# Kernel tuning notes

Hardware: AMD Instinct MI355X
Metric: run time of the kernel (lower is better)

The kernel has to match this reference:

```python
import jax, jax.numpy as jnp
import numpy as np
from jax import lax

T = 4096  # time length; conv widths 4094->1023->255->84 (even) so view(-1,30) works

def relu6(v):
    return jnp.clip(v, 0.0, 6.0)

def setup_inputs() -> dict:
    key = jax.random.key(0)
    ks = jax.random.split(key, 20)
    s = 0.25  # ~ torch default init scale for fan_in 16
    x = jax.random.normal(ks[0], (1, 1, 18, T), dtype=jnp.float32)
    # 4 stacked Linear(16,16) per cross-modal block: [Q, Kin, Vin, QKVout]
    cm1_W = jax.random.normal(ks[1], (4, 16, 16), dtype=jnp.float32) * s
    cm1_b = jax.random.normal(ks[2], (4, 16), dtype=jnp.float32) * s
    cm2_W = jax.random.normal(ks[3], (4, 16, 16), dtype=jnp.float32) * s
    cm2_b = jax.random.normal(ks[4], (4, 16), dtype=jnp.float32) * s
    cw0 = jax.random.normal(ks[5], (5, 1, 2, 3), dtype=jnp.float32) * 0.3
    cw1 = jax.random.normal(ks[6], (5, 5, 2, 4), dtype=jnp.float32) * 0.15
    cw2 = jax.random.normal(ks[7], (5, 5, 2, 4), dtype=jnp.float32) * 0.15
    cw3 = jax.random.normal(ks[8], (5, 5, 2, 4), dtype=jnp.float32) * 0.15
    cb = jax.random.normal(ks[9], (4, 5), dtype=jnp.float32) * 0.1
    fc1_W = jax.random.normal(ks[10], (15, 30), dtype=jnp.float32) * 0.18
    fc1_b = jax.random.normal(ks[11], (15,), dtype=jnp.float32) * 0.18
    fc2_W = jax.random.normal(ks[12], (2, 15), dtype=jnp.float32) * 0.25
    fc2_b = jax.random.normal(ks[13], (2,), dtype=jnp.float32) * 0.25
    return dict(x=x, cm1_W=cm1_W, cm1_b=cm1_b, cm2_W=cm2_W, cm2_b=cm2_b,
                cw0=cw0, cw1=cw1, cw2=cw2, cw3=cw3, cb=cb,
                fc1_W=fc1_W, fc1_b=fc1_b, fc2_W=fc2_W, fc2_b=fc2_b)

def _cm(wav_row, eeg2, W, b):
    # wav_row: [T], eeg2: [16, T]; W: [4,16,16], b: [4,16]
    wavP = wav_row[None, :] * eeg2          # [16, T]   (wav * eeg broadcast)
    mat = eeg2.T @ wavP                     # [T, T]
    wavP = wavP @ mat                       # [16, T]
    w = wavP.T                              # [T, 16]
    e = eeg2.T                              # [T, 16]
    Q = relu6(e @ W[0].T + b[0])            # [T, 16]
    K = relu6(w @ W[1].T + b[1])
    V = relu6(w @ W[2].T + b[2])
    # Softmax2d on [T,T,1,1] == softmax over axis 1 (per-row over keys)
    A = jax.nn.softmax(Q @ K.T, axis=1)     # [T, T]
    # Softmax2d on [T,16,1,1] == softmax over the 16 features per row
    S = jax.nn.softmax(A @ V, axis=1)       # [T, 16]
    out = relu6(S @ W[3].T + b[3])          # [T, 16]
    return out.T                            # [16, T]

def reference(x, cm1_W, cm1_b, cm2_W, cm2_b, cw0, cw1, cw2, cw3, cb,
              fc1_W, fc1_b, fc2_W, fc2_b):
    eeg2 = x[0, 0, 1:-1, :]                 # [16, T]
    wavA = _cm(x[0, 0, 0, :], eeg2, cm1_W, cm1_b)   # [16, T]
    wavB = _cm(x[0, 0, -1, :], eeg2, cm2_W, cm2_b)  # [16, T]
    y = jnp.concatenate([wavA, eeg2, wavB], axis=0)[None, None]  # [1,1,48,T]
    dn = ('NCHW', 'OIHW', 'NCHW')
    y = relu6(lax.conv_general_dilated(y, cw0, (2, 1), 'VALID', dimension_numbers=dn) + cb[0][None, :, None, None])
    y = relu6(lax.conv_general_dilated(y, cw1, (2, 4), 'VALID', dimension_numbers=dn) + cb[1][None, :, None, None])
    y = relu6(lax.conv_general_dilated(y, cw2, (2, 4), 'VALID', dimension_numbers=dn) + cb[2][None, :, None, None])
    y = relu6(lax.conv_general_dilated(y, cw3, (2, 3), 'VALID', dimension_numbers=dn) + cb[3][None, :, None, None])
    y = y.reshape(-1, 30)                   # [42, 30]
    h = jax.nn.sigmoid(y @ fc1_W.T + fc1_b) # [42, 15]
    out = jax.nn.softmax(h @ fc2_W.T + fc2_b, axis=1)  # [42, 2]
    return out
```

## Files before the change

kernel.cpp:

```cpp
#include <hip/hip_runtime.h>

#define TT 4096
#define KS 8

#define OFF_GPART 0
#define OFF_QH    32768
#define OFF_QL    98304
#define OFF_KH    163840
#define OFF_KL    229376
#define OFF_VT    294912
#define OFF_Y     360448
#define OFF_P     557056
#define OFF_C1    557056
#define OFF_C2    618496

typedef __attribute__((ext_vector_type(8))) short short8;
typedef __attribute__((ext_vector_type(4))) float f32x4;

__device__ __forceinline__ float relu6f(float v){ return fminf(fmaxf(v, 0.f), 6.f); }
__device__ __forceinline__ unsigned short f2bf(float f){
  unsigned int u = __float_as_uint(f);
  return (unsigned short)((u + 0x7FFFu + ((u>>16)&1u)) >> 16);
}
__device__ __forceinline__ float bf2f(unsigned short s){
  return __uint_as_float(((unsigned int)s)<<16);
}

__global__ __launch_bounds__(256) void k_gpart(const float* __restrict__ x, float* __restrict__ ws){
  const int b = blockIdx.x, tid = threadIdx.x;
  const int i = tid >> 4, j = tid & 15;
  const int t0 = b*64;
  const float4* ei4 = reinterpret_cast<const float4*>(x + (size_t)(1+i)*TT + t0);
  const float4* ej4 = reinterpret_cast<const float4*>(x + (size_t)(1+j)*TT + t0);
  const float4* wA4 = reinterpret_cast<const float4*>(x + t0);
  const float4* wB4 = reinterpret_cast<const float4*>(x + (size_t)17*TT + t0);
  float gA = 0.f, gB = 0.f;
  #pragma unroll 4
  for (int u = 0; u < 16; ++u){
    float4 a = ei4[u], c = ej4[u], wa = wA4[u], wb = wB4[u];
    float p0 = a.x*c.x, p1 = a.y*c.y, p2 = a.z*c.z, p3 = a.w*c.w;
    gA = fmaf(wa.x, p0, gA); gA = fmaf(wa.y, p1, gA); gA = fmaf(wa.z, p2, gA); gA = fmaf(wa.w, p3, gA);
    gB = fmaf(wb.x, p0, gB); gB = fmaf(wb.y, p1, gB); gB = fmaf(wb.z, p2, gB); gB = fmaf(wb.w, p3, gB);
  }
  ws[OFF_GPART + (size_t)tid*64 + b]         = gA;
  ws[OFF_GPART + (size_t)(256+tid)*64 + b]   = gB;
}

__global__ __launch_bounds__(128) void k_qkv(const float* __restrict__ x,
    const float* __restrict__ cm1W, const float* __restrict__ cm1b,
    const float* __restrict__ cm2W, const float* __restrict__ cm2b,
    float* __restrict__ ws){
  __shared__ float4 sG4[64];
  __shared__ float4 sW0[64], sW1[64], sW2[64];
  __shared__ float sB[48];
  const int b = blockIdx.x;
  const int cm = b >> 5;
  const int tid = threadIdx.x;
  {
    const float4* g4a = reinterpret_cast<const float4*>(ws + OFF_GPART + (size_t)(cm*256 + tid)*64);
    const float4* g4b = reinterpret_cast<const float4*>(ws + OFF_GPART + (size_t)(cm*256 + 128 + tid)*64);
    float g0 = 0.f, g1 = 0.f;
    #pragma unroll
    for (int u = 0; u < 16; ++u){
      float4 a = g4a[u], c = g4b[u];
      g0 += (a.x + a.y) + (a.z + a.w);
      g1 += (c.x + c.y) + (c.z + c.w);
    }
    ((float*)sG4)[tid]       = g0;
    ((float*)sG4)[tid + 128] = g1;
  }
  const float* W  = cm ? cm2W : cm1W;
  const float* Bb = cm ? cm2b : cm1b;
  ((float*)sW0)[tid]       = W[tid];
  ((float*)sW0)[tid + 128] = W[tid + 128];
  ((float*)sW1)[tid]       = W[256 + tid];
  ((float*)sW1)[tid + 128] = W[384 + tid];
  ((float*)sW2)[tid]       = W[512 + tid];
  ((float*)sW2)[tid + 128] = W[640 + tid];
  if (tid < 48) sB[tid] = Bb[tid];
  __syncthreads();

  const int t = (b & 31)*128 + tid;
  float e[16], p[16], w2[16];
  const float wav = x[(size_t)(cm ? 17 : 0)*TT + t];
  #pragma unroll
  for (int d = 0; d < 16; ++d){ e[d] = x[(size_t)(1+d)*TT + t]; p[d] = wav * e[d]; }

  #pragma unroll
  for (int c = 0; c < 16; ++c){
    float a = 0.f;
    #pragma unroll
    for (int dv = 0; dv < 4; ++dv){
      float4 gv = sG4[c*4+dv];
      a = fmaf(gv.x, p[4*dv+0], a); a = fmaf(gv.y, p[4*dv+1], a);
      a = fmaf(gv.z, p[4*dv+2], a); a = fmaf(gv.w, p[4*dv+3], a);
    }
    w2[c] = a;
  }
  float q[16], kk[16], vv[16];
  #pragma unroll
  for (int c = 0; c < 16; ++c){
    float aq = sB[c], ak = sB[16+c], av = sB[32+c];
    #pragma unroll
    for (int dv = 0; dv < 4; ++dv){
      float4 w0 = sW0[c*4+dv], w1 = sW1[c*4+dv], w3 = sW2[c*4+dv];
      aq = fmaf(w0.x, e[4*dv+0], aq);  aq = fmaf(w0.y, e[4*dv+1], aq);
      aq = fmaf(w0.z, e[4*dv+2], aq);  aq = fmaf(w0.w, e[4*dv+3], aq);
      ak = fmaf(w1.x, w2[4*dv+0], ak); ak = fmaf(w1.y, w2[4*dv+1], ak);
      ak = fmaf(w1.z, w2[4*dv+2], ak); ak = fmaf(w1.w, w2[4*dv+3], ak);
      av = fmaf(w3.x, w2[4*dv+0], av); av = fmaf(w3.y, w2[4*dv+1], av);
      av = fmaf(w3.z, w2[4*dv+2], av); av = fmaf(w3.w, w2[4*dv+3], av);
    }
    q[c] = relu6f(aq); kk[c] = relu6f(ak); vv[c] = relu6f(av);
  }
  unsigned short qhv[16], qlv[16], khv[16], klv[16];
  #pragma unroll
  for (int d = 0; d < 16; ++d){
    qhv[d] = f2bf(q[d]);  qlv[d] = f2bf(q[d]  - bf2f(qhv[d]));
    khv[d] = f2bf(kk[d]); klv[d] = f2bf(kk[d] - bf2f(khv[d]));
  }
  const size_t rowus = ((size_t)cm*TT + t)*16;
  unsigned int wq[8];
  #pragma unroll
  for (int xx = 0; xx < 8; ++xx) wq[xx] = (unsigned int)qhv[2*xx] | ((unsigned int)qhv[2*xx+1]<<16);
  ((uint4*)((unsigned short*)(ws+OFF_QH)+rowus))[0] = make_uint4(wq[0],wq[1],wq[2],wq[3]);
  ((uint4*)((unsigned short*)(ws+OFF_QH)+rowus))[1] = make_uint4(wq[4],wq[5],wq[6],wq[7]);
  #pragma unroll
  for (int xx = 0; xx < 8; ++xx) wq[xx] = (unsigned int)qlv[2*xx] | ((unsigned int)qlv[2*xx+1]<<16);
  ((uint4*)((unsigned short*)(ws+OFF_QL)+rowus))[0] = make_uint4(wq[0],wq[1],wq[2],wq[3]);
  ((uint4*)((unsigned short*)(ws+OFF_QL)+rowus))[1] = make_uint4(wq[4],wq[5],wq[6],wq[7]);
  #pragma unroll
  for (int xx = 0; xx < 8; ++xx) wq[xx] = (unsigned int)khv[2*xx] | ((unsigned int)khv[2*xx+1]<<16);
  ((uint4*)((unsigned short*)(ws+OFF_KH)+rowus))[0] = make_uint4(wq[0],wq[1],wq[2],wq[3]);
  ((uint4*)((unsigned short*)(ws+OFF_KH)+rowus))[1] = make_uint4(wq[4],wq[5],wq[6],wq[7]);
  #pragma unroll
  for (int xx = 0; xx < 8; ++xx) wq[xx] = (unsigned int)klv[2*xx] | ((unsigned int)klv[2*xx+1]<<16);
  ((uint4*)((unsigned short*)(ws+OFF_KL)+rowus))[0] = make_uint4(wq[0],wq[1],wq[2],wq[3]);
  ((uint4*)((unsigned short*)(ws+OFF_KL)+rowus))[1] = make_uint4(wq[4],wq[5],wq[6],wq[7]);
  unsigned short* vtp = (unsigned short*)(ws+OFF_VT) + (size_t)cm*16*TT;
  #pragma unroll
  for (int d = 0; d < 16; ++d) vtp[(size_t)d*TT + t] = f2bf(vv[d]);

  if (cm == 0){
    #pragma unroll
    for (int d = 0; d < 16; ++d) ws[OFF_Y + (size_t)(16+d)*TT + t] = e[d];
  }
}

__global__ __launch_bounds__(256) void k_attn_main(float* __restrict__ ws){
  const int unit = blockIdx.x*4 + (threadIdx.x >> 6);
  const int lane = threadIdx.x & 63;
  const int cm = unit >> 10;
  const int rem = unit & 1023;
  const int qt2 = rem >> 3;
  const int ks = rem & 7;
  const int i = lane & 15, g = lane >> 4;
  const int gb = (g & 1) * 8;

  const unsigned short* qh = (const unsigned short*)(ws + OFF_QH) + (size_t)cm*TT*16;
  const unsigned short* ql = (const unsigned short*)(ws + OFF_QL) + (size_t)cm*TT*16;
  const unsigned short* kh = (const unsigned short*)(ws + OFF_KH) + (size_t)cm*TT*16;
  const unsigned short* kl = (const unsigned short*)(ws + OFF_KL) + (size_t)cm*TT*16;
  const unsigned short* vt = (const unsigned short*)(ws + OFF_VT) + (size_t)cm*16*TT;
  const unsigned short* kbase = (g < 2) ? kh : kl;

  const int qA = qt2*32 + i, qB = qA + 16;
  const short8 b1A = *(const short8*)(qh + (size_t)qA*16 + gb);
  const short8 b2A = *(const short8*)(ql + (size_t)qA*16 + gb);
  const short8 b1B = *(const short8*)(qh + (size_t)qB*16 + gb);
  const short8 b2B = *(const short8*)(ql + (size_t)qB*16 + gb);

  const int key0 = ks*512;
  const int keyA = ((i>>2)<<3) + (i&3);
  f32x4 accA = {0.f,0.f,0.f,0.f}, accB = {0.f,0.f,0.f,0.f};
  float lsumA = 0.f, lsumB = 0.f;

  for (int t = 0; t < 16; ++t){
    const int k0 = key0 + t*32;
    const short8 a0 = *(const short8*)(kbase + ((size_t)(k0 + keyA))*16 + gb);
    const short8 a1 = *(const short8*)(kbase + ((size_t)(k0 + keyA + 4))*16 + gb);
    f32x4 d0A = {0.f,0.f,0.f,0.f}, d1A = {0.f,0.f,0.f,0.f};
    f32x4 d0B = {0.f,0.f,0.f,0.f}, d1B = {0.f,0.f,0.f,0.f};
    d0A = __builtin_amdgcn_mfma_f32_16x16x32_bf16(a0, b1A, d0A, 0,0,0);
    d0A = __builtin_amdgcn_mfma_f32_16x16x32_bf16(a0, b2A, d0A, 0,0,0);
    d1A = __builtin_amdgcn_mfma_f32_16x16x32_bf16(a1, b1A, d1A, 0,0,0);
    d1A = __builtin_amdgcn_mfma_f32_16x16x32_bf16(a1, b2A, d1A, 0,0,0);
    d0B = __builtin_amdgcn_mfma_f32_16x16x32_bf16(a0, b1B, d0B, 0,0,0);
    d0B = __builtin_amdgcn_mfma_f32_16x16x32_bf16(a0, b2B, d0B, 0,0,0);
    d1B = __builtin_amdgcn_mfma_f32_16x16x32_bf16(a1, b1B, d1B, 0,0,0);
    d1B = __builtin_amdgcn_mfma_f32_16x16x32_bf16(a1, b2B, d1B, 0,0,0);
    float p0A[4], p1A[4], p0B[4], p1B[4];
    #pragma unroll
    for (int r = 0; r < 4; ++r){
      p0A[r] = __expf(fminf(d0A[r],100.f) - 32.f); lsumA += p0A[r];
      p1A[r] = __expf(fminf(d1A[r],100.f) - 32.f); lsumA += p1A[r];
      p0B[r] = __expf(fminf(d0B[r],100.f) - 32.f); lsumB += p0B[r];
      p1B[r] = __expf(fminf(d1B[r],100.f) - 32.f); lsumB += p1B[r];
    }
    short8 paA, paB;
    #pragma unroll
    for (int r = 0; r < 4; ++r){
      paA[r]   = (short)f2bf(p0A[r]);
      paA[r+4] = (short)f2bf(p1A[r]);
      paB[r]   = (short)f2bf(p0B[r]);
      paB[r+4] = (short)f2bf(p1B[r]);
    }
    const short8 bv = *(const short8*)(vt + (size_t)i*TT + k0 + g*8);
    accA = __builtin_amdgcn_mfma_f32_16x16x32_bf16(paA, bv, accA, 0,0,0);
    accB = __builtin_amdgcn_mfma_f32_16x16x32_bf16(paB, bv, accB, 0,0,0);
  }
  lsumA += __shfl_xor(lsumA, 16);  lsumA += __shfl_xor(lsumA, 32);
  lsumB += __shfl_xor(lsumB, 16);  lsumB += __shfl_xor(lsumB, 32);
  float* Pb = ws + OFF_P + (size_t)((cm*KS + ks)*17)*TT;
  if (lane < 16){
    Pb[qt2*32 + lane]      = lsumA;
    Pb[qt2*32 + 16 + lane] = lsumB;
  }
  #pragma unroll
  for (int r = 0; r < 4; ++r){
    Pb[(size_t)(1 + i)*TT + qt2*32 + g*4 + r]      = accA[r];
    Pb[(size_t)(1 + i)*TT + qt2*32 + 16 + g*4 + r] = accB[r];
  }
}

__device__ __forceinline__ float sum8(const float* __restrict__ p){
  const size_t PL = (size_t)17*TT;
  float s0 = p[0],      s1 = p[PL],   s2 = p[2*PL], s3 = p[3*PL];
  float s4 = p[4*PL],   s5 = p[5*PL], s6 = p[6*PL], s7 = p[7*PL];
  return ((s0+s1)+(s2+s3)) + ((s4+s5)+(s6+s7));
}

__global__ __launch_bounds__(256) void k_attn_fin(
    const float* __restrict__ cm1W, const float* __restrict__ cm1b,
    const float* __restrict__ cm2W, const float* __restrict__ cm2b,
    float* __restrict__ ws){
  const int gid = blockIdx.x*256 + threadIdx.x;
  const int cm = gid >> 12;
  const int q = gid & 4095;
  const float* Pb = ws + OFF_P + (size_t)cm*KS*17*TT + q;
  const float lt = sum8(Pb);
  float a[16];
  #pragma unroll
  for (int d = 0; d < 16; ++d) a[d] = sum8(Pb + (size_t)(1+d)*TT);
  const float invl = 1.f/lt;
  float mx = -1e30f;
  #pragma unroll
  for (int d = 0; d < 16; ++d){ a[d] *= invl; mx = fmaxf(mx, a[d]); }
  float es = 0.f;
  #pragma unroll
  for (int d = 0; d < 16; ++d){ a[d] = __expf(a[d]-mx); es += a[d]; }
  const float invs = 1.f/es;
  const float* W  = cm ? cm2W : cm1W;
  const float* Bb = cm ? cm2b : cm1b;
  #pragma unroll
  for (int c = 0; c < 16; ++c){
    float o = 0.f;
    #pragma unroll
    for (int d = 0; d < 16; ++d) o = fmaf(W[768 + c*16 + d], a[d], o);
    o = relu6f(fmaf(o, invs, Bb[48 + c]));
    ws[OFF_Y + (size_t)((cm ? 32 : 0) + c)*TT + q] = o;
  }
}

__global__ __launch_bounds__(256) void k_conv01(const float* __restrict__ cw0,
    const float* __restrict__ cw1, const float* __restrict__ cb, float* __restrict__ ws){
  const int idx = blockIdx.x*256 + threadIdx.x;
  const int WO = 1023, HO = 12;
  if (idx >= 5*HO*WO) return;
  const int ow = idx % WO; int tmp = idx / WO;
  const int oh = tmp % HO; const int oc = tmp / HO;
  const float* y = ws + OFF_Y;
  float yp[4][7];
  #pragma unroll
  for (int r = 0; r < 4; ++r){
    const float* yr = y + (size_t)(4*oh + r)*TT + 4*ow;
    #pragma unroll
    for (int cx = 0; cx < 7; ++cx) yp[r][cx] = yr[cx];
  }
  float a = cb[5 + oc];
  #pragma unroll
  for (int ic = 0; ic < 5; ++ic){
    const float* w0 = cw0 + ic*6;
    const float* w1 = cw1 + ((oc*5+ic)*2)*4;
    #pragma unroll
    for (int kh = 0; kh < 2; ++kh){
      #pragma unroll
      for (int kw = 0; kw < 4; ++kw){
        float c0 = cb[ic];
        c0 = fmaf(w0[0], yp[2*kh][kw],   c0);
        c0 = fmaf(w0[1], yp[2*kh][kw+1], c0);
        c0 = fmaf(w0[2], yp[2*kh][kw+2], c0);
        c0 = fmaf(w0[3], yp[2*kh+1][kw],   c0);
        c0 = fmaf(w0[4], yp[2*kh+1][kw+1], c0);
        c0 = fmaf(w0[5], yp[2*kh+1][kw+2], c0);
        c0 = relu6f(c0);
        a = fmaf(w1[kh*4+kw], c0, a);
      }
    }
  }
  ws[OFF_C1 + idx] = relu6f(a);
}

__global__ __launch_bounds__(256) void k_conv2(const float* __restrict__ cw2,
    const float* __restrict__ cb, float* __restrict__ ws){
  const int idx = blockIdx.x*256 + threadIdx.x;
  if (idx >= 5*6*255) return;
  const int ow = idx % 255; int tmp = idx/255;
  const int oh = tmp % 6; const int oc = tmp/6;
  const float* c1 = ws + OFF_C1;
  float a = cb[10 + oc];
  #pragma unroll
  for (int ic = 0; ic < 5; ++ic)
    #pragma unroll
    for (int kh = 0; kh < 2; ++kh)
      #pragma unroll
      for (int kw = 0; kw < 4; ++kw)
        a = fmaf(cw2[((oc*5+ic)*2+kh)*4+kw], c1[(size_t)(ic*12 + 2*oh+kh)*1023 + 4*ow+kw], a);
  ws[OFF_C2 + idx] = relu6f(a);
}

__global__ __launch_bounds__(256) void k_tail(
    const float* __restrict__ cw3, const float* __restrict__ cb,
    const float* __restrict__ fc1W, const float* __restrict__ fc1b,
    const float* __restrict__ fc2W, const float* __restrict__ fc2b,
    const float* __restrict__ ws, float* __restrict__ out){
  __shared__ float c2[5*6*255];
  __shared__ float c3[5*3*84];
  __shared__ float hsm[42*15];
  const int tid = threadIdx.x;
  {
    const float4* src4 = reinterpret_cast<const float4*>(ws + OFF_C2);
    float4* c24 = reinterpret_cast<float4*>(c2);
    for (int i = tid; i < 1912; i += 256) c24[i] = src4[i];
    if (tid < 2) c2[7648 + tid] = ws[OFF_C2 + 7648 + tid];
  }
  __syncthreads();
  for (int idx = tid; idx < 5*3*84; idx += 256){
    const int ow = idx % 84; int tmp = idx/84;
    const int oh = tmp % 3; const int oc = tmp/3;
    float a = cb[15 + oc];
    #pragma unroll
    for (int ic = 0; ic < 5; ++ic)
      #pragma unroll
      for (int kh = 0; kh < 2; ++kh)
        #pragma unroll
        for (int kw = 0; kw < 4; ++kw)
          a = fmaf(cw3[((oc*5+ic)*2+kh)*4+kw], c2[(ic*6 + 2*oh+kh)*255 + 3*ow+kw], a);
    c3[idx] = relu6f(a);
  }
  __syncthreads();
  for (int i = tid; i < 630; i += 256){
    const int s = i / 15, kx = i % 15;
    const float* row = c3 + s*30;
    float a = fc1b[kx];
    #pragma unroll
    for (int n = 0; n < 30; ++n) a = fmaf(fc1W[kx*30+n], row[n], a);
    hsm[i] = 1.f/(1.f + __expf(-a));
  }
  __syncthreads();
  if (tid < 42){
    const float* h = hsm + tid*15;
    float l0 = fc2b[0], l1 = fc2b[1];
    #pragma unroll
    for (int kx = 0; kx < 15; ++kx){
      l0 = fmaf(fc2W[kx],    h[kx], l0);
      l1 = fmaf(fc2W[15+kx], h[kx], l1);
    }
    float mx = fmaxf(l0, l1);
    float e0 = __expf(l0-mx), e1 = __expf(l1-mx);
    float s = e0 + e1;
    out[tid*2]   = e0/s;
    out[tid*2+1] = e1/s;
  }
}

extern "C" void kernel_launch(void* const* d_in, const int* in_sizes, int n_in,
                              void* d_out, int out_size, void* d_ws, size_t ws_size,
                              hipStream_t stream){
  const float* x    = (const float*)d_in[0];
  const float* cm1W = (const float*)d_in[1];
  const float* cm1b = (const float*)d_in[2];
  const float* cm2W = (const float*)d_in[3];
  const float* cm2b = (const float*)d_in[4];
  const float* cw0  = (const float*)d_in[5];
  const float* cw1  = (const float*)d_in[6];
  const float* cw2  = (const float*)d_in[7];
  const float* cw3  = (const float*)d_in[8];
  const float* cb   = (const float*)d_in[9];
  const float* fc1W = (const float*)d_in[10];
  const float* fc1b = (const float*)d_in[11];
  const float* fc2W = (const float*)d_in[12];
  const float* fc2b = (const float*)d_in[13];
  float* ws  = (float*)d_ws;
  float* out = (float*)d_out;

  k_gpart    <<<dim3(64),  dim3(256), 0, stream>>>(x, ws);
  k_qkv      <<<dim3(64),  dim3(128), 0, stream>>>(x, cm1W, cm1b, cm2W, cm2b, ws);
  k_attn_main<<<dim3(512), dim3(256), 0, stream>>>(ws);
  k_attn_fin <<<dim3(32),  dim3(256), 0, stream>>>(cm1W, cm1b, cm2W, cm2b, ws);
  k_conv01   <<<dim3(240), dim3(256), 0, stream>>>(cw0, cw1, cb, ws);
  k_conv2    <<<dim3(30),  dim3(256), 0, stream>>>(cw2, cb, ws);
  k_tail     <<<dim3(1),   dim3(256), 0, stream>>>(cw3, cb, fc1W, fc1b, fc2W, fc2b, ws, out);
}
```

Before: 61.85 us.

## Spread attention finalize over 512 blocks with shared-memory partial reduction

The attention finalize kernel used 32 blocks, one thread per query, each summing 17x8 split-K partials and computing all 16 outputs serially. It now launches 512 blocks where 16 threads per query each reduce one feature row into shared memory, then each thread produces one output channel. The aim is more parallelism and memory-level parallelism on a kernel that only occupied a few CUs. In exchange it adds a block barrier and redundant softmax work per thread, and the loads are only 16-wide coalesced.

```diff
diff --git a/kernel.cpp b/kernel.cpp
--- a/kernel.cpp
+++ b/kernel.cpp
@@ -223,43 +223,50 @@
   }
 }
 
-__device__ __forceinline__ float sum8(const float* __restrict__ p){
-  const size_t PL = (size_t)17*TT;
-  float s0 = p[0],      s1 = p[PL],   s2 = p[2*PL], s3 = p[3*PL];
-  float s4 = p[4*PL],   s5 = p[5*PL], s6 = p[6*PL], s7 = p[7*PL];
-  return ((s0+s1)+(s2+s3)) + ((s4+s5)+(s6+s7));
-}
-
-__global__ __launch_bounds__(256) void k_attn_fin(
+__global__ __launch_bounds__(256) void k_attn_fin2(
     const float* __restrict__ cm1W, const float* __restrict__ cm1b,
     const float* __restrict__ cm2W, const float* __restrict__ cm2b,
     float* __restrict__ ws){
-  const int gid = blockIdx.x*256 + threadIdx.x;
-  const int cm = gid >> 12;
-  const int q = gid & 4095;
-  const float* Pb = ws + OFF_P + (size_t)cm*KS*17*TT + q;
-  const float lt = sum8(Pb);
+  __shared__ float sA[16][16];
+  __shared__ float sL[16];
+  const int b = blockIdx.x;
+  const int cm = b >> 8;
+  const int qb = b & 255;
+  const int tid = threadIdx.x;
+  const int p = tid >> 4, qo = tid & 15;
+  const int q = qb*16 + qo;
+  const float* Pc = ws + OFF_P + (size_t)cm*KS*17*TT;
+  const size_t PL = (size_t)17*TT;
+  {
+    const float* src = Pc + (size_t)(1+p)*TT + q;
+    float s0 = src[0],    s1 = src[PL],   s2 = src[2*PL], s3 = src[3*PL];
+    float s4 = src[4*PL], s5 = src[5*PL], s6 = src[6*PL], s7 = src[7*PL];
+    sA[p][qo] = ((s0+s1)+(s2+s3)) + ((s4+s5)+(s6+s7));
+    if (p == 0){
+      const float* sl = Pc + q;
+      float t0 = sl[0],    t1 = sl[PL],   t2 = sl[2*PL], t3 = sl[3*PL];
+      float t4 = sl[4*PL], t5 = sl[5*PL], t6 = sl[6*PL], t7 = sl[7*PL];
+      sL[qo] = ((t0+t1)+(t2+t3)) + ((t4+t5)+(t6+t7));
+    }
+  }
+  __syncthreads();
+  const int c = p;
+  const float invl = 1.f / sL[qo];
   float a[16];
-  #pragma unroll
-  for (int d = 0; d < 16; ++d) a[d] = sum8(Pb + (size_t)(1+d)*TT);
-  const float invl = 1.f/lt;
   float mx = -1e30f;
   #pragma unroll
-  for (int d = 0; d < 16; ++d){ a[d] *= invl; mx = fmaxf(mx, a[d]); }
+  for (int d = 0; d < 16; ++d){ a[d] = sA[d][qo] * invl; mx = fmaxf(mx, a[d]); }
   float es = 0.f;
   #pragma unroll
   for (int d = 0; d < 16; ++d){ a[d] = __expf(a[d]-mx); es += a[d]; }
   const float invs = 1.f/es;
   const float* W  = cm ? cm2W : cm1W;
   const float* Bb = cm ? cm2b : cm1b;
-  #pragma unroll
-  for (int c = 0; c < 16; ++c){
-    float o = 0.f;
-    #pragma unroll
-    for (int d = 0; d < 16; ++d) o = fmaf(W[768 + c*16 + d], a[d], o);
-    o = relu6f(fmaf(o, invs, Bb[48 + c]));
-    ws[OFF_Y + (size_t)((cm ? 32 : 0) + c)*TT + q] = o;
-  }
+  float o = 0.f;
+  #pragma unroll
+  for (int d = 0; d < 16; ++d) o = fmaf(W[768 + c*16 + d], a[d], o);
+  o = relu6f(fmaf(o, invs, Bb[48 + c]));
+  ws[OFF_Y + (size_t)((cm ? 32 : 0) + c)*TT + q] = o;
 }
 
 __global__ __launch_bounds__(256) void k_conv01(const float* __restrict__ cw0,
@@ -397,7 +404,7 @@
   k_gpart    <<<dim3(64),  dim3(256), 0, stream>>>(x, ws);
   k_qkv      <<<dim3(64),  dim3(128), 0, stream>>>(x, cm1W, cm1b, cm2W, cm2b, ws);
   k_attn_main<<<dim3(512), dim3(256), 0, stream>>>(ws);
-  k_attn_fin <<<dim3(32),  dim3(256), 0, stream>>>(cm1W, cm1b, cm2W, cm2b, ws);
+  k_attn_fin2<<<dim3(512), dim3(256), 0, stream>>>(cm1W, cm1b, cm2W, cm2b, ws);
   k_conv01   <<<dim3(240), dim3(256), 0, stream>>>(cw0, cw1, cb, ws);
   k_conv2    <<<dim3(30),  dim3(256), 0, stream>>>(cw2, cb, ws);
   k_tail     <<<dim3(1),   dim3(256), 0, stream>>>(cw3, cb, fc1W, fc1b, fc2W, fc2b, ws, out);
```

Result: faster. 54.08 us, median of 2 (-12.6%).
